# Kernel tuning notes

Measured on AMD Instinct MI355X. Metric: run time of the kernel, lower is better.

Reference implementation:

```python
import jax, jax.numpy as jnp
import numpy as np

N_NODES = 50000
N_EDGES = 800000
IN_FEATS = 256
OUT_FEATS = 32
NUM_HEADS = 8
NEG_SLOPE = 0.2


def setup_inputs() -> dict:
    key = jax.random.key(0)
    k_feat, k_src, k_dst, k_w, k_al, k_ar = jax.random.split(key, 6)
    feat = jax.random.normal(k_feat, (N_NODES, IN_FEATS), dtype=jnp.float32)
    src = jax.random.randint(k_src, (N_EDGES,), 0, N_NODES)
    dst = jax.random.randint(k_dst, (N_EDGES,), 0, N_NODES)
    # fc weight, stored as [in, H*F] so projection is feat @ W
    W = jax.random.normal(k_w, (IN_FEATS, NUM_HEADS * OUT_FEATS), dtype=jnp.float32) * 0.05
    attn_l = jax.random.normal(k_al, (NUM_HEADS, OUT_FEATS), dtype=jnp.float32) * 0.1
    attn_r = jax.random.normal(k_ar, (NUM_HEADS, OUT_FEATS), dtype=jnp.float32) * 0.1
    bias = jnp.zeros((NUM_HEADS, OUT_FEATS), dtype=jnp.float32)
    return {"feat": feat, "W": W, "attn_l": attn_l, "attn_r": attn_r,
            "bias": bias, "src": src, "dst": dst}


def reference(feat, W, attn_l, attn_r, bias, src, dst):
    N = feat.shape[0]
    H, F = attn_l.shape
    # node projection: [N, H, F]
    h = (feat @ W).reshape(N, H, F)
    # per-node attention logits (source code uses feat_src for both el and er)
    el = jnp.einsum('nhf,hf->nh', h, attn_l)  # [N, H]
    er = jnp.einsum('nhf,hf->nh', h, attn_r)  # [N, H]
    # per-edge logit: u_add_v then LeakyReLU
    e = el[src] + er[dst]                      # [E, H]
    e = jnp.where(e > 0, e, NEG_SLOPE * e)
    # edge softmax normalized over incoming edges of each dst node
    m = jax.ops.segment_max(e, dst, num_segments=N)   # [N, H], -inf for 0-deg
    ex = jnp.exp(e - m[dst])                           # [E, H]
    s = jax.ops.segment_sum(ex, dst, num_segments=N)   # [N, H]
    a = ex / s[dst]                                     # [E, H]
    # weighted scatter-sum aggregation: u_mul_e -> sum
    msg = h[src] * a[:, :, None]                        # [E, H, F]
    rst = jax.ops.segment_sum(msg, dst, num_segments=N)  # [N, H, F]
    rst = rst + bias[None, :, :]
    return rst
```

## Files before the change

### kernel.cpp

```cpp
#include <hip/hip_runtime.h>
#include <math.h>

#define NN 50000
#define NE 800000
#define IN_F 256
#define HF 256
#define NH 8
#define NEG_SLOPE 0.2f
#define CAP 64

#define GEMM_BLOCKS 782
#define EDGE_BLOCKS 3125
#define ELR_BLOCKS 12500
#define AGG_BLOCKS 3125
#define ZERO_BLOCKS 196

typedef short bf16x8 __attribute__((ext_vector_type(8)));
typedef float f32x16 __attribute__((ext_vector_type(16)));

__device__ __forceinline__ unsigned short f2bf(float x) {
    unsigned u = __float_as_uint(x);
    u += 0x7FFF + ((u >> 16) & 1);
    return (unsigned short)(u >> 16);
}
__device__ __forceinline__ float bf2f(unsigned short b) {
    return __uint_as_float(((unsigned)b) << 16);
}

__global__ __launch_bounds__(256) void wconv_zero_kernel(const float* __restrict__ W,
                                                         unsigned short* __restrict__ Wb,
                                                         int* __restrict__ cnt) {
    int bid = blockIdx.x;
    if (bid < 256) {
        int e = bid * 256 + threadIdx.x;
        int k = e >> 8, n = e & 255;
        float x = W[e];
        int kt = k >> 5, kk = k & 31;
        Wb[((size_t)(kt * 256 + n)) * 32 + kk] = f2bf(x);
    } else {
        int i = (bid - 256) * 256 + threadIdx.x;
        if (i < NN) cnt[i] = 0;
    }
}

__global__ void fill2_kernel(const int* __restrict__ src, const int* __restrict__ dst,
                             int* __restrict__ cnt, unsigned short* __restrict__ slots) {
    int e = blockIdx.x * 256 + threadIdx.x;
    if (e < NE) {
        int d = dst[e];
        int pos = atomicAdd(&cnt[d], 1);
        if (pos < CAP) slots[(size_t)d * CAP + pos] = (unsigned short)src[e];
    }
}

__global__ __launch_bounds__(256) void gemm_kernel(const float* __restrict__ feat,
                                                   const unsigned short* __restrict__ Wb,
                                                   unsigned short* __restrict__ h, int M) {
    __shared__ __align__(16) unsigned short As_hi[2][64][40];
    __shared__ __align__(16) unsigned short As_lo[2][64][40];

    const int tid = threadIdx.x;
    const int lane = tid & 63;
    const int wid = tid >> 6;
    const int bm = blockIdx.x * 64;

    const int arow = tid >> 2;
    const int achk = tid & 3;
    const int grow = bm + arow;
    const int crow = (grow < M) ? grow : 0;
    const float* ap = feat + (size_t)crow * IN_F + achk * 8;

    f32x16 acc[2][2];
    #pragma unroll
    for (int mi = 0; mi < 2; ++mi)
        #pragma unroll
        for (int ni = 0; ni < 2; ++ni)
            #pragma unroll
            for (int r = 0; r < 16; ++r) acc[mi][ni][r] = 0.f;

    const int khalf = lane >> 5;
    const int nbase = wid * 64 + (lane & 31);

    float4 cur0 = *(const float4*)(ap);
    float4 cur1 = *(const float4*)(ap + 4);

    for (int kt = 0; kt < 8; ++kt) {
        const int buf = kt & 1;
        float4 nxt0, nxt1;
        if (kt < 7) {
            nxt0 = *(const float4*)(ap + (kt + 1) * 32);
            nxt1 = *(const float4*)(ap + (kt + 1) * 32 + 4);
        }
        bf16x8 bh[2][2];
        #pragma unroll
        for (int ksc = 0; ksc < 2; ++ksc)
            #pragma unroll
            for (int ni = 0; ni < 2; ++ni)
                bh[ksc][ni] = *(const bf16x8*)(Wb
                    + ((size_t)(kt * 256) + nbase + ni * 32) * 32
                    + (ksc * 2 + khalf) * 8);

        float xs[8] = {cur0.x, cur0.y, cur0.z, cur0.w, cur1.x, cur1.y, cur1.z, cur1.w};
        unsigned hi2[4], lo2[4];
        #pragma unroll
        for (int p = 0; p < 4; ++p) {
            unsigned short h0 = f2bf(xs[2 * p]), h1 = f2bf(xs[2 * p + 1]);
            unsigned short l0 = f2bf(xs[2 * p] - bf2f(h0));
            unsigned short l1 = f2bf(xs[2 * p + 1] - bf2f(h1));
            hi2[p] = (unsigned)h0 | ((unsigned)h1 << 16);
            lo2[p] = (unsigned)l0 | ((unsigned)l1 << 16);
        }
        *(int4*)&As_hi[buf][arow][achk * 8] = make_int4(hi2[0], hi2[1], hi2[2], hi2[3]);
        *(int4*)&As_lo[buf][arow][achk * 8] = make_int4(lo2[0], lo2[1], lo2[2], lo2[3]);
        __syncthreads();

        #pragma unroll
        for (int ksc = 0; ksc < 2; ++ksc) {
            const int kchunk = ksc * 2 + khalf;
            bf16x8 ah[2], av[2];
            #pragma unroll
            for (int mi = 0; mi < 2; ++mi) {
                int r = mi * 32 + (lane & 31);
                ah[mi] = *(const bf16x8*)&As_hi[buf][r][kchunk * 8];
                av[mi] = *(const bf16x8*)&As_lo[buf][r][kchunk * 8];
            }
            #pragma unroll
            for (int mi = 0; mi < 2; ++mi)
                #pragma unroll
                for (int ni = 0; ni < 2; ++ni) {
                    acc[mi][ni] = __builtin_amdgcn_mfma_f32_32x32x16_bf16(ah[mi], bh[ksc][ni], acc[mi][ni], 0, 0, 0);
                    acc[mi][ni] = __builtin_amdgcn_mfma_f32_32x32x16_bf16(av[mi], bh[ksc][ni], acc[mi][ni], 0, 0, 0);
                }
        }
        cur0 = nxt0;
        cur1 = nxt1;
    }

    #pragma unroll
    for (int mi = 0; mi < 2; ++mi)
        #pragma unroll
        for (int ni = 0; ni < 2; ++ni)
            #pragma unroll
            for (int r = 0; r < 16; ++r) {
                int row = mi * 32 + (r & 3) + 8 * (r >> 2) + 4 * (lane >> 5);
                int col = wid * 64 + ni * 32 + (lane & 31);
                int gr = bm + row;
                if (gr < M) h[(size_t)gr * HF + col] = f2bf(acc[mi][ni][r]);
            }
}

__global__ __launch_bounds__(256) void elr_kernel(const unsigned short* __restrict__ h,
                                                  const float* __restrict__ al,
                                                  const float* __restrict__ ar,
                                                  float* __restrict__ el,
                                                  float* __restrict__ er) {
    int node = blockIdx.x * 4 + (threadIdx.x >> 6);
    if (node >= NN) return;
    int lane = threadIdx.x & 63;
    short4 hv = *(const short4*)&h[(size_t)node * HF + lane * 4];
    float h0 = bf2f((unsigned short)hv.x), h1 = bf2f((unsigned short)hv.y);
    float h2 = bf2f((unsigned short)hv.z), h3 = bf2f((unsigned short)hv.w);
    float4 alv = *(const float4*)&al[lane * 4];
    float4 arv = *(const float4*)&ar[lane * 4];
    float pl = h0 * alv.x + h1 * alv.y + h2 * alv.z + h3 * alv.w;
    float pr = h0 * arv.x + h1 * arv.y + h2 * arv.z + h3 * arv.w;
    #pragma unroll
    for (int off = 1; off < 8; off <<= 1) {
        pl += __shfl_xor(pl, off);
        pr += __shfl_xor(pr, off);
    }
    if ((lane & 7) == 0) {
        el[node * NH + (lane >> 3)] = pl;
        er[node * NH + (lane >> 3)] = pr;
    }
}

__global__ __launch_bounds__(256) void agg_kernel(const unsigned short* __restrict__ h,
                                                  const float* __restrict__ el,
                                                  const float* __restrict__ er,
                                                  const int* __restrict__ cnt,
                                                  const unsigned short* __restrict__ slots,
                                                  const float* __restrict__ bias,
                                                  float* __restrict__ out) {
    int wv = blockIdx.x * 4 + (threadIdx.x >> 6);
    int lane = threadIdx.x & 63;
    int eg = lane >> 3;
    int fg = lane & 7;
    int e2 = (lane >> 5) & 1, e1 = (lane >> 4) & 1, e0 = (lane >> 3) & 1;
    int col = fg * 32 + eg * 4;
    float4 bv = *(const float4*)&bias[col];

    int4 deg4 = *(const int4*)&cnt[wv * 4];

    #pragma unroll 1
    for (int t = 0; t < 4; ++t) {
        int node = wv * 4 + t;
        int deg = (t == 0) ? deg4.x : (t == 1) ? deg4.y : (t == 2) ? deg4.z : deg4.w;
        deg = deg < CAP ? deg : CAP;
        const unsigned short* sl = slots + (size_t)node * CAP;
        float er_mine = er[(size_t)node * NH + fg];

        float ssum = 0.f;
        float acc[32];
        #pragma unroll
        for (int j = 0; j < 32; ++j) acc[j] = 0.f;

        for (int i0 = 0; i0 < deg; i0 += 16) {
            int idxA = i0 + eg;
            int idxB = i0 + 8 + eg;
            bool vA = idxA < deg, vB = idxB < deg;
            int sA = sl[vA ? idxA : 0];
            int sB = sl[vB ? idxB : 0];
            float eA = el[(size_t)sA * NH + fg] + er_mine;
            float eB = el[(size_t)sB * NH + fg] + er_mine;
            eA = eA > 0.f ? eA : NEG_SLOPE * eA;
            eB = eB > 0.f ? eB : NEG_SLOPE * eB;
            float pA = vA ? __expf(eA) : 0.f;
            float pB = vB ? __expf(eB) : 0.f;
            ssum += pA + pB;
            const unsigned short* hpA = h + (size_t)sA * HF + fg * 32;
            const unsigned short* hpB = h + (size_t)sB * HF + fg * 32;
            bf16x8 va[4], vb[4];
            #pragma unroll
            for (int c = 0; c < 4; ++c) { va[c] = *(const bf16x8*)(hpA + c * 8); }
            #pragma unroll
            for (int c = 0; c < 4; ++c) { vb[c] = *(const bf16x8*)(hpB + c * 8); }
            #pragma unroll
            for (int c = 0; c < 4; ++c)
                #pragma unroll
                for (int k = 0; k < 8; ++k) {
                    acc[c * 8 + k] = fmaf(bf2f((unsigned short)va[c][k]), pA, acc[c * 8 + k]);
                    acc[c * 8 + k] = fmaf(bf2f((unsigned short)vb[c][k]), pB, acc[c * 8 + k]);
                }
        }

        ssum += __shfl_xor(ssum, 8);
        ssum += __shfl_xor(ssum, 16);
        ssum += __shfl_xor(ssum, 32);
        float inv_s = (ssum > 0.f) ? 1.f / ssum : 0.f;

        float t16[16];
        #pragma unroll
        for (int j = 0; j < 16; ++j) {
            float keep = e2 ? acc[16 + j] : acc[j];
            float send = e2 ? acc[j] : acc[16 + j];
            t16[j] = keep + __shfl_xor(send, 32);
        }
        float t8[8];
        #pragma unroll
        for (int j = 0; j < 8; ++j) {
            float keep = e1 ? t16[8 + j] : t16[j];
            float send = e1 ? t16[j] : t16[8 + j];
            t8[j] = keep + __shfl_xor(send, 16);
        }
        float t4[4];
        #pragma unroll
        for (int j = 0; j < 4; ++j) {
            float keep = e0 ? t8[4 + j] : t8[j];
            float send = e0 ? t8[j] : t8[4 + j];
            t4[j] = keep + __shfl_xor(send, 8);
        }

        float4 o = make_float4(fmaf(t4[0], inv_s, bv.x), fmaf(t4[1], inv_s, bv.y),
                               fmaf(t4[2], inv_s, bv.z), fmaf(t4[3], inv_s, bv.w));
        *(float4*)&out[(size_t)node * HF + col] = o;
    }
}

extern "C" void kernel_launch(void* const* d_in, const int* in_sizes, int n_in,
                              void* d_out, int out_size, void* d_ws, size_t ws_size,
                              hipStream_t stream) {
    const float* feat = (const float*)d_in[0];
    const float* W    = (const float*)d_in[1];
    const float* al   = (const float*)d_in[2];
    const float* ar   = (const float*)d_in[3];
    const float* bias = (const float*)d_in[4];
    const int*   src  = (const int*)d_in[5];
    const int*   dst  = (const int*)d_in[6];
    float* out = (float*)d_out;

    char* ws = (char*)d_ws;
    size_t off = 0;
    unsigned short* h = (unsigned short*)(ws + off);     off += (size_t)NN * HF * 2;
    float* el = (float*)(ws + off);                      off += (size_t)NN * NH * 4;
    float* er = (float*)(ws + off);                      off += (size_t)NN * NH * 4;
    int* cnt = (int*)(ws + off);                         off += (size_t)NN * 4;
    unsigned short* slots = (unsigned short*)(ws + off); off += (size_t)NN * CAP * 2;
    unsigned short* Wb = (unsigned short*)(ws + off);    off += (size_t)IN_F * HF * 2;

    wconv_zero_kernel<<<256 + ZERO_BLOCKS, 256, 0, stream>>>(W, Wb, cnt);
    fill2_kernel<<<EDGE_BLOCKS, 256, 0, stream>>>(src, dst, cnt, slots);
    gemm_kernel<<<GEMM_BLOCKS, 256, 0, stream>>>(feat, Wb, h, NN);
    elr_kernel<<<ELR_BLOCKS, 256, 0, stream>>>(h, al, ar, el, er);
    agg_kernel<<<AGG_BLOCKS, 256, 0, stream>>>(h, el, er, cnt, slots, bias, out);
}
```

Before: 159.5 us.

## Store projected features head-major and aggregate one head per block

Changes the projection output, el and er to a head-major layout ([head][node][32]). The aggregation kernel now launches one block per (node chunk, head), so each head's 3.2MB feature slice is reused from cache across its gathers. Each lane gathers 8 bytes instead of 64, and the big 32-accumulator cross-lane transpose becomes small shuffle reductions. In exchange, the edge slot lists and exp logits are recomputed once per head (8x), and the gathers are narrower and less coalesced.

```diff
diff --git a/kernel.cpp b/kernel.cpp
--- a/kernel.cpp
+++ b/kernel.cpp
@@ -12,7 +12,7 @@
 #define GEMM_BLOCKS 782
 #define EDGE_BLOCKS 3125
 #define ELR_BLOCKS 12500
-#define AGG_BLOCKS 3125
+#define AGG_CHUNKS 782
 #define ZERO_BLOCKS 196
 
 typedef short bf16x8 __attribute__((ext_vector_type(8)));
@@ -55,7 +55,7 @@
 
 __global__ __launch_bounds__(256) void gemm_kernel(const float* __restrict__ feat,
                                                    const unsigned short* __restrict__ Wb,
-                                                   unsigned short* __restrict__ h, int M) {
+                                                   unsigned short* __restrict__ h2, int M) {
     __shared__ __align__(16) unsigned short As_hi[2][64][40];
     __shared__ __align__(16) unsigned short As_lo[2][64][40];
 
@@ -139,131 +139,116 @@
     #pragma unroll
     for (int mi = 0; mi < 2; ++mi)
         #pragma unroll
-        for (int ni = 0; ni < 2; ++ni)
+        for (int ni = 0; ni < 2; ++ni) {
+            const int hd = wid * 2 + ni;
             #pragma unroll
             for (int r = 0; r < 16; ++r) {
                 int row = mi * 32 + (r & 3) + 8 * (r >> 2) + 4 * (lane >> 5);
-                int col = wid * 64 + ni * 32 + (lane & 31);
+                int colin = lane & 31;
                 int gr = bm + row;
-                if (gr < M) h[(size_t)gr * HF + col] = f2bf(acc[mi][ni][r]);
+                if (gr < M) h2[((size_t)hd * NN + gr) * 32 + colin] = f2bf(acc[mi][ni][r]);
             }
-}
-
-__global__ __launch_bounds__(256) void elr_kernel(const unsigned short* __restrict__ h,
+        }
+}
+
+__global__ __launch_bounds__(256) void elr_kernel(const unsigned short* __restrict__ h2,
                                                   const float* __restrict__ al,
                                                   const float* __restrict__ ar,
-                                                  float* __restrict__ el,
-                                                  float* __restrict__ er) {
+                                                  float* __restrict__ el2,
+                                                  float* __restrict__ er2) {
     int node = blockIdx.x * 4 + (threadIdx.x >> 6);
     if (node >= NN) return;
     int lane = threadIdx.x & 63;
-    short4 hv = *(const short4*)&h[(size_t)node * HF + lane * 4];
+    int hd = lane >> 3, fo = (lane & 7) * 4;
+    short4 hv = *(const short4*)&h2[((size_t)hd * NN + node) * 32 + fo];
     float h0 = bf2f((unsigned short)hv.x), h1 = bf2f((unsigned short)hv.y);
-    float h2 = bf2f((unsigned short)hv.z), h3 = bf2f((unsigned short)hv.w);
+    float h2f = bf2f((unsigned short)hv.z), h3 = bf2f((unsigned short)hv.w);
     float4 alv = *(const float4*)&al[lane * 4];
     float4 arv = *(const float4*)&ar[lane * 4];
-    float pl = h0 * alv.x + h1 * alv.y + h2 * alv.z + h3 * alv.w;
-    float pr = h0 * arv.x + h1 * arv.y + h2 * arv.z + h3 * arv.w;
+    float pl = h0 * alv.x + h1 * alv.y + h2f * alv.z + h3 * alv.w;
+    float pr = h0 * arv.x + h1 * arv.y + h2f * arv.z + h3 * arv.w;
     #pragma unroll
     for (int off = 1; off < 8; off <<= 1) {
         pl += __shfl_xor(pl, off);
         pr += __shfl_xor(pr, off);
     }
     if ((lane & 7) == 0) {
-        el[node * NH + (lane >> 3)] = pl;
-        er[node * NH + (lane >> 3)] = pr;
-    }
-}
-
-__global__ __launch_bounds__(256) void agg_kernel(const unsigned short* __restrict__ h,
-                                                  const float* __restrict__ el,
-                                                  const float* __restrict__ er,
-                                                  const int* __restrict__ cnt,
-                                                  const unsigned short* __restrict__ slots,
-                                                  const float* __restrict__ bias,
-                                                  float* __restrict__ out) {
-    int wv = blockIdx.x * 4 + (threadIdx.x >> 6);
-    int lane = threadIdx.x & 63;
-    int eg = lane >> 3;
-    int fg = lane & 7;
-    int e2 = (lane >> 5) & 1, e1 = (lane >> 4) & 1, e0 = (lane >> 3) & 1;
-    int col = fg * 32 + eg * 4;
-    float4 bv = *(const float4*)&bias[col];
-
-    int4 deg4 = *(const int4*)&cnt[wv * 4];
+        el2[(size_t)hd * NN + node] = pl;
+        er2[(size_t)hd * NN + node] = pr;
+    }
+}
+
+__global__ __launch_bounds__(256) void agg2_kernel(const unsigned short* __restrict__ h2,
+                                                   const float* __restrict__ el2,
+                                                   const float* __restrict__ er2,
+                                                   const int* __restrict__ cnt,
+                                                   const unsigned short* __restrict__ slots,
+                                                   const float* __restrict__ bias,
+                                                   float* __restrict__ out) {
+    const int bid = blockIdx.x;
+    const int hd = bid & 7;
+    const int chunk = bid >> 3;
+    const int wid = threadIdx.x >> 6;
+    const int lane = threadIdx.x & 63;
+    const int eg = lane >> 3;
+    const int fq = lane & 7;
+    const int node0 = chunk * 64 + wid * 16;
+
+    const unsigned short* hh = h2 + (size_t)hd * NN * 32;
+    const float* elh = el2 + (size_t)hd * NN;
+    const float* erh = er2 + (size_t)hd * NN;
+    float4 bv = *(const float4*)&bias[hd * 32 + fq * 4];
 
     #pragma unroll 1
-    for (int t = 0; t < 4; ++t) {
-        int node = wv * 4 + t;
-        int deg = (t == 0) ? deg4.x : (t == 1) ? deg4.y : (t == 2) ? deg4.z : deg4.w;
+    for (int t = 0; t < 16; ++t) {
+        int node = node0 + t;
+        if (node >= NN) return;
+        int deg = cnt[node];
         deg = deg < CAP ? deg : CAP;
         const unsigned short* sl = slots + (size_t)node * CAP;
-        float er_mine = er[(size_t)node * NH + fg];
+        float ern = erh[node];
 
         float ssum = 0.f;
-        float acc[32];
-        #pragma unroll
-        for (int j = 0; j < 32; ++j) acc[j] = 0.f;
+        float a0 = 0.f, a1 = 0.f, a2 = 0.f, a3 = 0.f;
 
         for (int i0 = 0; i0 < deg; i0 += 16) {
-            int idxA = i0 + eg;
-            int idxB = i0 + 8 + eg;
-            bool vA = idxA < deg, vB = idxB < deg;
-            int sA = sl[vA ? idxA : 0];
-            int sB = sl[vB ? idxB : 0];
-            float eA = el[(size_t)sA * NH + fg] + er_mine;
-            float eB = el[(size_t)sB * NH + fg] + er_mine;
+            int iA = i0 + eg;
+            int iB = i0 + 8 + eg;
+            bool vA = iA < deg, vB = iB < deg;
+            int sA = sl[vA ? iA : 0];
+            int sB = sl[vB ? iB : 0];
+            float eA = elh[sA] + ern;
+            float eB = elh[sB] + ern;
             eA = eA > 0.f ? eA : NEG_SLOPE * eA;
             eB = eB > 0.f ? eB : NEG_SLOPE * eB;
             float pA = vA ? __expf(eA) : 0.f;
             float pB = vB ? __expf(eB) : 0.f;
             ssum += pA + pB;
-            const unsigned short* hpA = h + (size_t)sA * HF + fg * 32;
-            const unsigned short* hpB = h + (size_t)sB * HF + fg * 32;
-            bf16x8 va[4], vb[4];
-            #pragma unroll
-            for (int c = 0; c < 4; ++c) { va[c] = *(const bf16x8*)(hpA + c * 8); }
-            #pragma unroll
-            for (int c = 0; c < 4; ++c) { vb[c] = *(const bf16x8*)(hpB + c * 8); }
-            #pragma unroll
-            for (int c = 0; c < 4; ++c)
-                #pragma unroll
-                for (int k = 0; k < 8; ++k) {
-                    acc[c * 8 + k] = fmaf(bf2f((unsigned short)va[c][k]), pA, acc[c * 8 + k]);
-                    acc[c * 8 + k] = fmaf(bf2f((unsigned short)vb[c][k]), pB, acc[c * 8 + k]);
-                }
-        }
-
-        ssum += __shfl_xor(ssum, 8);
-        ssum += __shfl_xor(ssum, 16);
-        ssum += __shfl_xor(ssum, 32);
+            short4 ha = *(const short4*)(hh + (size_t)sA * 32 + fq * 4);
+            short4 hb = *(const short4*)(hh + (size_t)sB * 32 + fq * 4);
+            a0 = fmaf(bf2f((unsigned short)ha.x), pA, a0);
+            a1 = fmaf(bf2f((unsigned short)ha.y), pA, a1);
+            a2 = fmaf(bf2f((unsigned short)ha.z), pA, a2);
+            a3 = fmaf(bf2f((unsigned short)ha.w), pA, a3);
+            a0 = fmaf(bf2f((unsigned short)hb.x), pB, a0);
+            a1 = fmaf(bf2f((unsigned short)hb.y), pB, a1);
+            a2 = fmaf(bf2f((unsigned short)hb.z), pB, a2);
+            a3 = fmaf(bf2f((unsigned short)hb.w), pB, a3);
+        }
+
+        ssum += __shfl_xor(ssum, 8);  a0 += __shfl_xor(a0, 8);  a1 += __shfl_xor(a1, 8);
+        a2 += __shfl_xor(a2, 8);      a3 += __shfl_xor(a3, 8);
+        ssum += __shfl_xor(ssum, 16); a0 += __shfl_xor(a0, 16); a1 += __shfl_xor(a1, 16);
+        a2 += __shfl_xor(a2, 16);     a3 += __shfl_xor(a3, 16);
+        ssum += __shfl_xor(ssum, 32); a0 += __shfl_xor(a0, 32); a1 += __shfl_xor(a1, 32);
+        a2 += __shfl_xor(a2, 32);     a3 += __shfl_xor(a3, 32);
+
         float inv_s = (ssum > 0.f) ? 1.f / ssum : 0.f;
-
-        float t16[16];
-        #pragma unroll
-        for (int j = 0; j < 16; ++j) {
-            float keep = e2 ? acc[16 + j] : acc[j];
-            float send = e2 ? acc[j] : acc[16 + j];
-            t16[j] = keep + __shfl_xor(send, 32);
-        }
-        float t8[8];
-        #pragma unroll
-        for (int j = 0; j < 8; ++j) {
-            float keep = e1 ? t16[8 + j] : t16[j];
-            float send = e1 ? t16[j] : t16[8 + j];
-            t8[j] = keep + __shfl_xor(send, 16);
-        }
-        float t4[4];
-        #pragma unroll
-        for (int j = 0; j < 4; ++j) {
-            float keep = e0 ? t8[4 + j] : t8[j];
-            float send = e0 ? t8[j] : t8[4 + j];
-            t4[j] = keep + __shfl_xor(send, 8);
-        }
-
-        float4 o = make_float4(fmaf(t4[0], inv_s, bv.x), fmaf(t4[1], inv_s, bv.y),
-                               fmaf(t4[2], inv_s, bv.z), fmaf(t4[3], inv_s, bv.w));
-        *(float4*)&out[(size_t)node * HF + col] = o;
+        if (eg == 0) {
+            float4 o = make_float4(fmaf(a0, inv_s, bv.x), fmaf(a1, inv_s, bv.y),
+                                   fmaf(a2, inv_s, bv.z), fmaf(a3, inv_s, bv.w));
+            *(float4*)&out[(size_t)node * HF + hd * 32 + fq * 4] = o;
+        }
     }
 }
 
@@ -281,16 +266,16 @@
 
     char* ws = (char*)d_ws;
     size_t off = 0;
-    unsigned short* h = (unsigned short*)(ws + off);     off += (size_t)NN * HF * 2;
-    float* el = (float*)(ws + off);                      off += (size_t)NN * NH * 4;
-    float* er = (float*)(ws + off);                      off += (size_t)NN * NH * 4;
+    unsigned short* h2 = (unsigned short*)(ws + off);    off += (size_t)NN * HF * 2;
+    float* el2 = (float*)(ws + off);                     off += (size_t)NN * NH * 4;
+    float* er2 = (float*)(ws + off);                     off += (size_t)NN * NH * 4;
     int* cnt = (int*)(ws + off);                         off += (size_t)NN * 4;
     unsigned short* slots = (unsigned short*)(ws + off); off += (size_t)NN * CAP * 2;
     unsigned short* Wb = (unsigned short*)(ws + off);    off += (size_t)IN_F * HF * 2;
 
     wconv_zero_kernel<<<256 + ZERO_BLOCKS, 256, 0, stream>>>(W, Wb, cnt);
     fill2_kernel<<<EDGE_BLOCKS, 256, 0, stream>>>(src, dst, cnt, slots);
-    gemm_kernel<<<GEMM_BLOCKS, 256, 0, stream>>>(feat, Wb, h, NN);
-    elr_kernel<<<ELR_BLOCKS, 256, 0, stream>>>(h, al, ar, el, er);
-    agg_kernel<<<AGG_BLOCKS, 256, 0, stream>>>(h, el, er, cnt, slots, bias, out);
-}
+    gemm_kernel<<<GEMM_BLOCKS, 256, 0, stream>>>(feat, Wb, h2, NN);
+    elr_kernel<<<ELR_BLOCKS, 256, 0, stream>>>(h2, al, ar, el2, er2);
+    agg2_kernel<<<AGG_CHUNKS * 8, 256, 0, stream>>>(h2, el2, er2, cnt, slots, bias, out);
+}
```

After: 219.5 us, median of 2. 1.38x slower.
